# Performance work log

Hardware: AMD Instinct MI355X
Metric: run time of the kernel (lower is better)

Reference implementation:

```python
import jax, jax.numpy as jnp
import numpy as np

D_IN = 512
D_OUT = 512
EPS = 1e-5


def setup_inputs() -> dict:
    key = jax.random.key(0)
    ks = jax.random.split(key, 6)
    B, T = 256, D_OUT + 1  # T includes CLS token (dropped in forward)
    x = jax.random.normal(ks[0], (B, T, D_IN), dtype=jnp.float32)
    s = 1.0 / np.sqrt(D_IN)
    W1 = jax.random.uniform(ks[1], (D_IN, D_IN), jnp.float32, -s, s)
    b1 = jax.random.uniform(ks[2], (D_IN,), jnp.float32, -s, s)
    gamma = jnp.ones((D_IN,), jnp.float32)
    beta = jnp.zeros((D_IN,), jnp.float32)
    Wout = jax.random.uniform(ks[3], (D_OUT, D_IN), jnp.float32, -s, s)  # stacked per-column Linear(d_in,1) weights
    bout = jax.random.uniform(ks[4], (D_OUT,), jnp.float32, -s, s)
    return {"x": x, "W1": W1, "b1": b1, "gamma": gamma, "beta": beta,
            "Wout": Wout, "bout": bout}


def reference(x, W1, b1, gamma, beta, Wout, bout):
    h = x[:, :-1]                              # drop CLS: [B, d_out, d_in]
    h = jnp.einsum('btd,ed->bte', h, W1) + b1  # linear1
    mu = jnp.mean(h, axis=-1, keepdims=True)
    var = jnp.mean(jnp.square(h - mu), axis=-1, keepdims=True)
    h = (h - mu) * jax.lax.rsqrt(var + EPS) * gamma + beta  # LayerNorm
    h = jax.nn.relu(h)
    # per-column head: out[:, t] = h[:, t] @ Wout[t] + bout[t]
    out = jnp.einsum('btd,td->bt', h, Wout) + bout  # [B, d_out]
    return out
```

## Files before the change

### kernel.cpp

```cpp
#include <hip/hip_runtime.h>


#define DIN     512
#define BK      32
#define MT      64
#define THREADS 512
#define NCHUNK  (DIN / BK)
#define ASTR    40
#define BSTR    32

typedef __attribute__((ext_vector_type(8))) short bf16x8;
typedef __attribute__((ext_vector_type(4))) float f32x4;

__device__ __forceinline__ short f2bf(float f) {
    unsigned u = __float_as_uint(f);
    u = u + 0x7fffu + ((u >> 16) & 1u);
    return (short)(u >> 16);
}

__device__ __forceinline__ void gload_lds16(const void* g, void* l) {
    __builtin_amdgcn_global_load_lds(
        (const __attribute__((address_space(1))) unsigned int*)g,
        (__attribute__((address_space(3))) unsigned int*)l,
        16, 0, 0);
}

__global__ void cvt_w1_kernel(const float* __restrict__ w, short* __restrict__ o) {
    int i = blockIdx.x * blockDim.x + threadIdx.x;
    float4 v = ((const float4*)w)[i];
    short4 s;
    s.x = f2bf(v.x); s.y = f2bf(v.y); s.z = f2bf(v.z); s.w = f2bf(v.w);
    ((short4*)o)[i] = s;
}

template<bool WS>
__global__ __launch_bounds__(THREADS, 2)
void fused_head_kernel(const float* __restrict__ x,
                       const float* __restrict__ W1f,
                       const short* __restrict__ W1h,
                       const float* __restrict__ b1,
                       const float* __restrict__ gamma,
                       const float* __restrict__ beta,
                       const float* __restrict__ Wout,
                       const float* __restrict__ bout,
                       float* __restrict__ out) {
    __shared__ __align__(16) short As[MT * ASTR];
    __shared__ __align__(16) short Bs[DIN * BSTR];
    __shared__ float redS[MT][4];
    __shared__ float redQ[MT][4];
    __shared__ float meanA[MT];
    __shared__ float rstdA[MT];

    const int tid  = threadIdx.x;
    const int w    = tid >> 6;
    const int lane = tid & 63;
    const int q    = lane >> 4;
    const int l15  = lane & 15;
    const int rg   = w >> 2;
    const int cg   = w & 3;

    const int m0 = blockIdx.x * MT;
    const int bb = m0 >> 9;
    const int t0 = m0 & 511;
    const float* xbase = x + (size_t)(bb * 513 + t0) * DIN;

    const int ar = tid >> 3;
    const int ak = (tid & 7) * 4;

    const short* bG = W1h + (size_t)(w * 64 + (lane >> 2)) * DIN + (lane & 3) * 8;
    short* bL = Bs + (w * 64) * BSTR;

    f32x4 acc[2][8];
#pragma unroll
    for (int i = 0; i < 2; ++i)
#pragma unroll
        for (int j = 0; j < 8; ++j)
            acc[i][j] = (f32x4){0.f, 0.f, 0.f, 0.f};

    float4 aReg = *(const float4*)(xbase + ar * DIN + ak);

    for (int c = 0; c < NCHUNK; ++c) {
        __syncthreads();
        {
            short4 a4;
            a4.x = f2bf(aReg.x); a4.y = f2bf(aReg.y);
            a4.z = f2bf(aReg.z); a4.w = f2bf(aReg.w);
            *(short4*)(&As[ar * ASTR + ak]) = a4;
        }
        if (WS) {
#pragma unroll
            for (int j = 0; j < 4; ++j)
                gload_lds16(bG + (size_t)(j * 16) * DIN + c * BK,
                            bL + j * 16 * BSTR);
        } else {
            const float* src = W1f + (size_t)tid * DIN + c * BK;
#pragma unroll
            for (int p = 0; p < 8; ++p) {
                float4 v = *(const float4*)(src + p * 4);
                short4 s4;
                s4.x = f2bf(v.x); s4.y = f2bf(v.y);
                s4.z = f2bf(v.z); s4.w = f2bf(v.w);
                *(short4*)(&Bs[tid * BSTR + p * 4]) = s4;
            }
        }
        __syncthreads();

        if (c + 1 < NCHUNK)
            aReg = *(const float4*)(xbase + ar * DIN + (c + 1) * BK + ak);

        bf16x8 af[2], bfr[8];
        const short* Ap = As + (rg * 32 + l15) * ASTR + q * 8;
        af[0] = *(const bf16x8*)Ap;
        af[1] = *(const bf16x8*)(Ap + 16 * ASTR);
        const short* Bp = Bs + (cg * 128 + l15) * BSTR + q * 8;
#pragma unroll
        for (int tj = 0; tj < 8; ++tj)
            bfr[tj] = *(const bf16x8*)(Bp + tj * 16 * BSTR);
#pragma unroll
        for (int ti = 0; ti < 2; ++ti)
#pragma unroll
            for (int tj = 0; tj < 8; ++tj)
                acc[ti][tj] = __builtin_amdgcn_mfma_f32_16x16x32_bf16(
                    af[ti], bfr[tj], acc[ti][tj], 0, 0, 0);
    }

    float b1v[8], gv[8], bv[8];
    const int cb = cg * 128 + l15;
#pragma unroll
    for (int tj = 0; tj < 8; ++tj) {
        int col = cb + tj * 16;
        b1v[tj] = b1[col];
        gv[tj]  = gamma[col];
        bv[tj]  = beta[col];
    }

#pragma unroll
    for (int ti = 0; ti < 2; ++ti)
#pragma unroll
        for (int r = 0; r < 4; ++r) {
            int row = rg * 32 + ti * 16 + q * 4 + r;
            float s = 0.f, s2 = 0.f;
#pragma unroll
            for (int tj = 0; tj < 8; ++tj) {
                float v = acc[ti][tj][r] + b1v[tj];
                s += v; s2 += v * v;
            }
#pragma unroll
            for (int m = 1; m < 16; m <<= 1) {
                s  += __shfl_xor(s,  m, 64);
                s2 += __shfl_xor(s2, m, 64);
            }
            if (l15 == 0) { redS[row][cg] = s; redQ[row][cg] = s2; }
        }
    __syncthreads();
    if (tid < MT) {
        float s  = redS[tid][0] + redS[tid][1] + redS[tid][2] + redS[tid][3];
        float s2 = redQ[tid][0] + redQ[tid][1] + redQ[tid][2] + redQ[tid][3];
        float mean = s * (1.f / DIN);
        float var  = s2 * (1.f / DIN) - mean * mean;
        meanA[tid] = mean;
        rstdA[tid] = rsqrtf(fmaxf(var, 0.f) + 1e-5f);
    }
    __syncthreads();

#pragma unroll
    for (int ti = 0; ti < 2; ++ti)
#pragma unroll
        for (int r = 0; r < 4; ++r) {
            int row = rg * 32 + ti * 16 + q * 4 + r;
            float mean = meanA[row], rs = rstdA[row];
            const float* wrow = Wout + (size_t)(t0 + row) * DIN + cb;
            float s = 0.f;
#pragma unroll
            for (int tj = 0; tj < 8; ++tj) {
                float v = acc[ti][tj][r] + b1v[tj];
                v = (v - mean) * rs * gv[tj] + bv[tj];
                v = fmaxf(v, 0.f);
                s += v * wrow[tj * 16];
            }
#pragma unroll
            for (int m = 1; m < 16; m <<= 1)
                s += __shfl_xor(s, m, 64);
            if (l15 == 0) redS[row][cg] = s;
        }
    __syncthreads();
    if (tid < MT)
        out[m0 + tid] = redS[tid][0] + redS[tid][1] + redS[tid][2] + redS[tid][3]
                        + bout[t0 + tid];
}

extern "C" void kernel_launch(void* const* d_in, const int* in_sizes, int n_in,
                              void* d_out, int out_size, void* d_ws, size_t ws_size,
                              hipStream_t stream) {
    const float* x     = (const float*)d_in[0];
    const float* W1    = (const float*)d_in[1];
    const float* b1    = (const float*)d_in[2];
    const float* gamma = (const float*)d_in[3];
    const float* beta  = (const float*)d_in[4];
    const float* Wout  = (const float*)d_in[5];
    const float* bout  = (const float*)d_in[6];
    float* out = (float*)d_out;

    const int M = 256 * 512;
    dim3 grid(M / MT), block(THREADS);

    if (ws_size >= (size_t)(DIN * DIN) * sizeof(short)) {
        short* W1h = (short*)d_ws;
        cvt_w1_kernel<<<DIN * DIN / (256 * 4), 256, 0, stream>>>(W1, W1h);
        fused_head_kernel<true><<<grid, block, 0, stream>>>(
            x, W1, W1h, b1, gamma, beta, Wout, bout, out);
    } else {
        fused_head_kernel<false><<<grid, block, 0, stream>>>(
            x, W1, nullptr, b1, gamma, beta, Wout, bout, out);
    }
}
```

Before: 435.1 us.

## Double-buffer LDS tiles, swizzle B layout, and double block tile to 128 rows

Doubles the M tile to 128 rows with 1024 threads per block, so each staged W1 chunk is reused across twice as many rows. A and B tiles are double-buffered in LDS, so the next chunk's loads are issued before the current chunk's MFMAs, and the per-iteration sync count drops from two to one. The B tile in LDS gets an XOR swizzle to reduce bank conflicts on the fragment reads. The trade-off is fewer blocks per CU, since LDS use and block size grow and the occupancy hint of 2 is dropped, which may cut latency hiding.

```diff
diff --git a/kernel.cpp b/kernel.cpp
--- a/kernel.cpp
+++ b/kernel.cpp
@@ -3,11 +3,11 @@
 
 #define DIN     512
 #define BK      32
-#define MT      64
-#define THREADS 512
+#define MT      128
+#define THREADS 1024
 #define NCHUNK  (DIN / BK)
 #define ASTR    40
-#define BSTR    32
+#define BROW    32
 
 typedef __attribute__((ext_vector_type(8))) short bf16x8;
 typedef __attribute__((ext_vector_type(4))) float f32x4;
@@ -33,8 +33,25 @@
     ((short4*)o)[i] = s;
 }
 
+__device__ __forceinline__ void stage_b_f32(short* bsb, const float* W1f,
+                                            int c, int tid) {
+    if (tid < DIN) {
+        const float* src = W1f + (size_t)tid * DIN + c * BK;
+        const int rp = tid & 3;
+#pragma unroll
+        for (int g = 0; g < 4; ++g) {
+            float4 v0 = *(const float4*)(src + g * 8);
+            float4 v1 = *(const float4*)(src + g * 8 + 4);
+            bf16x8 s;
+            s[0] = f2bf(v0.x); s[1] = f2bf(v0.y); s[2] = f2bf(v0.z); s[3] = f2bf(v0.w);
+            s[4] = f2bf(v1.x); s[5] = f2bf(v1.y); s[6] = f2bf(v1.z); s[7] = f2bf(v1.w);
+            *(bf16x8*)(bsb + tid * BROW + ((g ^ rp) * 8)) = s;
+        }
+    }
+}
+
 template<bool WS>
-__global__ __launch_bounds__(THREADS, 2)
+__global__ __launch_bounds__(THREADS)
 void fused_head_kernel(const float* __restrict__ x,
                        const float* __restrict__ W1f,
                        const short* __restrict__ W1h,
@@ -44,8 +61,8 @@
                        const float* __restrict__ Wout,
                        const float* __restrict__ bout,
                        float* __restrict__ out) {
-    __shared__ __align__(16) short As[MT * ASTR];
-    __shared__ __align__(16) short Bs[DIN * BSTR];
+    __shared__ __align__(16) short As[2][MT * ASTR];
+    __shared__ __align__(16) short Bs[2][DIN * BROW];
     __shared__ float redS[MT][4];
     __shared__ float redQ[MT][4];
     __shared__ float meanA[MT];
@@ -67,8 +84,9 @@
     const int ar = tid >> 3;
     const int ak = (tid & 7) * 4;
 
-    const short* bG = W1h + (size_t)(w * 64 + (lane >> 2)) * DIN + (lane & 3) * 8;
-    short* bL = Bs + (w * 64) * BSTR;
+    const int r16 = lane >> 2;
+    const int kg  = (lane & 3) ^ (r16 & 3);
+    const short* bG = W1h + (size_t)(w * 32 + r16) * DIN + kg * 8;
 
     f32x4 acc[2][8];
 #pragma unroll
@@ -78,50 +96,49 @@
             acc[i][j] = (f32x4){0.f, 0.f, 0.f, 0.f};
 
     float4 aReg = *(const float4*)(xbase + ar * DIN + ak);
+    if (WS) {
+        gload_lds16(bG,            &Bs[0][(w * 32) * BROW]);
+        gload_lds16(bG + 16 * DIN, &Bs[0][(w * 32 + 16) * BROW]);
+    } else {
+        stage_b_f32(&Bs[0][0], W1f, 0, tid);
+    }
+    {
+        short4 a4;
+        a4.x = f2bf(aReg.x); a4.y = f2bf(aReg.y);
+        a4.z = f2bf(aReg.z); a4.w = f2bf(aReg.w);
+        *(short4*)(&As[0][ar * ASTR + ak]) = a4;
+    }
+    aReg = *(const float4*)(xbase + ar * DIN + BK + ak);
 
     for (int c = 0; c < NCHUNK; ++c) {
+        const int cur = c & 1, nxt = cur ^ 1;
         __syncthreads();
-        {
+        if (c + 1 < NCHUNK) {
+            if (WS) {
+                const short* g = bG + (size_t)(c + 1) * BK;
+                gload_lds16(g,            &Bs[nxt][(w * 32) * BROW]);
+                gload_lds16(g + 16 * DIN, &Bs[nxt][(w * 32 + 16) * BROW]);
+            } else {
+                stage_b_f32(&Bs[nxt][0], W1f, c + 1, tid);
+            }
             short4 a4;
             a4.x = f2bf(aReg.x); a4.y = f2bf(aReg.y);
             a4.z = f2bf(aReg.z); a4.w = f2bf(aReg.w);
-            *(short4*)(&As[ar * ASTR + ak]) = a4;
-        }
-        if (WS) {
-#pragma unroll
-            for (int j = 0; j < 4; ++j)
-                gload_lds16(bG + (size_t)(j * 16) * DIN + c * BK,
-                            bL + j * 16 * BSTR);
-        } else {
-            const float* src = W1f + (size_t)tid * DIN + c * BK;
-#pragma unroll
-            for (int p = 0; p < 8; ++p) {
-                float4 v = *(const float4*)(src + p * 4);
-                short4 s4;
-                s4.x = f2bf(v.x); s4.y = f2bf(v.y);
-                s4.z = f2bf(v.z); s4.w = f2bf(v.w);
-                *(short4*)(&Bs[tid * BSTR + p * 4]) = s4;
-            }
-        }
-        __syncthreads();
-
-        if (c + 1 < NCHUNK)
-            aReg = *(const float4*)(xbase + ar * DIN + (c + 1) * BK + ak);
-
-        bf16x8 af[2], bfr[8];
-        const short* Ap = As + (rg * 32 + l15) * ASTR + q * 8;
+            *(short4*)(&As[nxt][ar * ASTR + ak]) = a4;
+            if (c + 2 < NCHUNK)
+                aReg = *(const float4*)(xbase + ar * DIN + (c + 2) * BK + ak);
+        }
+        bf16x8 af[2];
+        const short* Ap = &As[cur][(rg * 32 + l15) * ASTR + q * 8];
         af[0] = *(const bf16x8*)Ap;
         af[1] = *(const bf16x8*)(Ap + 16 * ASTR);
-        const short* Bp = Bs + (cg * 128 + l15) * BSTR + q * 8;
-#pragma unroll
-        for (int tj = 0; tj < 8; ++tj)
-            bfr[tj] = *(const bf16x8*)(Bp + tj * 16 * BSTR);
-#pragma unroll
-        for (int ti = 0; ti < 2; ++ti)
-#pragma unroll
-            for (int tj = 0; tj < 8; ++tj)
-                acc[ti][tj] = __builtin_amdgcn_mfma_f32_16x16x32_bf16(
-                    af[ti], bfr[tj], acc[ti][tj], 0, 0, 0);
+        const short* Bp = &Bs[cur][(cg * 128 + l15) * BROW + ((q ^ (l15 & 3)) * 8)];
+#pragma unroll
+        for (int tj = 0; tj < 8; ++tj) {
+            bf16x8 bf = *(const bf16x8*)(Bp + tj * 16 * BROW);
+            acc[0][tj] = __builtin_amdgcn_mfma_f32_16x16x32_bf16(af[0], bf, acc[0][tj], 0, 0, 0);
+            acc[1][tj] = __builtin_amdgcn_mfma_f32_16x16x32_bf16(af[1], bf, acc[1][tj], 0, 0, 0);
+        }
     }
 
     float b1v[8], gv[8], bv[8];
```

After: 446.2 us. 2.6% more time.
